# Kernel optimization log

Measured on AMD Instinct MI355X. Metric: run time of the kernel, lower is better.

Reference implementation:

```python
import jax, jax.numpy as jnp
import numpy as np

N = 100000
E = 1600000
IN_FT = 128
HID = 128
LEAK = 0.2  # GATConv default negative_slope


def _glorot(key, shape):
    fan_in, fan_out = shape[0], shape[-1]
    s = float(np.sqrt(6.0 / (fan_in + fan_out)))
    return jax.random.uniform(key, shape, jnp.float32, -s, s)


def setup_inputs() -> dict:
    key = jax.random.key(0)
    ks = jax.random.split(key, 12)
    return {
        "x": jax.random.normal(ks[0], (N, IN_FT), jnp.float32),
        "edge_index": jax.random.randint(ks[1], (2, E), 0, N, dtype=jnp.int64) if jax.config.jax_enable_x64 else jax.random.randint(ks[1], (2, E), 0, N, dtype=jnp.int32),
        "edge_weight": jax.random.uniform(ks[2], (E,), jnp.float32),
        "W1": _glorot(ks[3], (IN_FT, HID)),
        "a_src1": _glorot(ks[4], (HID, 1))[:, 0],
        "a_dst1": _glorot(ks[5], (HID, 1))[:, 0],
        "b1": jnp.zeros((HID,), jnp.float32),
        "W2": _glorot(ks[6], (HID, HID)),
        "a_src2": _glorot(ks[7], (HID, 1))[:, 0],
        "a_dst2": _glorot(ks[8], (HID, 1))[:, 0],
        "b2": jnp.zeros((HID,), jnp.float32),
    }


def _gat_layer(h_in, src, dst, n, W, a_src, a_dst, b):
    # h: [N, HID] dense projection
    h = h_in @ W
    # per-node attention halves, then edge-wise combine (classic GAT, 1 head)
    s_src = h @ a_src  # [N]
    s_dst = h @ a_dst  # [N]
    e = jax.nn.leaky_relu(s_src[src] + s_dst[dst], LEAK)  # [E+N]
    # softmax over incoming edges of each dst node (self-loops guarantee non-empty)
    m = jax.ops.segment_max(e, dst, num_segments=n)
    ex = jnp.exp(e - m[dst])
    denom = jax.ops.segment_sum(ex, dst, num_segments=n)
    alpha = ex / denom[dst]
    # scatter-aggregate messages alpha_ij * h_j
    out = jax.ops.segment_sum(alpha[:, None] * h[src], dst, num_segments=n)
    return out + b


def reference(x, edge_index, edge_weight, W1, a_src1, a_dst1, b1, W2, a_src2, a_dst2, b2):
    # edge_weight is accepted but unused: PyG GATConv with edge_dim=None ignores edge_attr.
    n = x.shape[0]
    loops = jnp.arange(n, dtype=edge_index.dtype)  # add_self_loops=True
    src = jnp.concatenate([edge_index[0], loops])
    dst = jnp.concatenate([edge_index[1], loops])
    x1 = jnp.tanh(_gat_layer(x, src, dst, n, W1, a_src1, a_dst1, b1))
    # dropout: identity in eval mode
    x2 = _gat_layer(x1, src, dst, n, W2, a_src2, a_dst2, b2)
    # update='max': elementwise max over stacked layer outputs
    return jnp.maximum(x1, x2)
```

## Files before the change

### kernel.cpp

```cpp
#include <hip/hip_runtime.h>
#include <math.h>

#define NN 100000
#define NE 1600000
#define EE 1700000
#define HD 128
#define NH (NN*HD)

#define BSH 8
#define NBUK 391
#define CAP 6144
#define EPB 4096
#define P1B ((EE + EPB - 1) / EPB)
#define GEMMB 1563

typedef _Float16 f16x8 __attribute__((ext_vector_type(8)));
typedef float    f32x4 __attribute__((ext_vector_type(4)));

__device__ __forceinline__ float fast_tanh(float x) {
    float e = __expf(2.f * x);
    return 1.f - 2.f * __builtin_amdgcn_rcpf(e + 1.f);
}

__global__ void wt12_kernel(const float* __restrict__ W1, const float* __restrict__ W2,
                            _Float16* __restrict__ Wt1, _Float16* __restrict__ Wt2) {
    int b = blockIdx.x;
    const float* W = (b < 64) ? W1 : W2;
    _Float16* Wt   = (b < 64) ? Wt1 : Wt2;
    int e = (b & 63) * 256 + threadIdx.x;
    int k = e >> 7, n = e & 127;
    Wt[n*HD + k] = (_Float16)W[e];
}

__launch_bounds__(256) __global__
void gemm_part_kernel(const float* __restrict__ A, const _Float16* __restrict__ Wt,
                      _Float16* __restrict__ H, const float* __restrict__ a_src,
                      const float* __restrict__ a_dst, float* __restrict__ s_src,
                      float* __restrict__ s_dst,
                      const int* __restrict__ ei, int* __restrict__ bucketCount,
                      unsigned* __restrict__ stage) {
    __shared__ __align__(16) char smem[HD*HD*2 + HD*8];
    int bid = blockIdx.x;
    int t = threadIdx.x;

    if (bid < GEMMB) {
        _Float16* Wl = (_Float16*)smem;
        float* asl = (float*)(smem + HD*HD*2);
        float* adl = asl + HD;
        #pragma unroll
        for (int i = 0; i < 8; ++i) {
            int f = t + 256*i;
            int n = f >> 4, slot = f & 15;
            int phys = n*16 + (slot ^ (n & 7));
            *(float4*)(Wl + (size_t)phys*8) = ((const float4*)Wt)[f];
        }
        if (t < HD) { asl[t] = a_src[t]; adl[t] = a_dst[t]; }
        __syncthreads();

        int wave = t >> 6, lane = t & 63;
        int row0 = bid*64 + wave*16;
        int h8   = lane >> 4;
        int col  = lane & 15;
        int arow = row0 + col; if (arow >= NN) arow = NN - 1;
        const float* Af = A + (size_t)arow*HD + h8*8;

        f32x4 acc[8];
        #pragma unroll
        for (int i = 0; i < 8; ++i) acc[i] = (f32x4){0.f,0.f,0.f,0.f};

        #pragma unroll
        for (int step = 0; step < 4; ++step) {
            float4 fa = *(const float4*)(Af + step*32);
            float4 fb = *(const float4*)(Af + step*32 + 4);
            f16x8 a = { (_Float16)fa.x, (_Float16)fa.y, (_Float16)fa.z, (_Float16)fa.w,
                        (_Float16)fb.x, (_Float16)fb.y, (_Float16)fb.z, (_Float16)fb.w };
            #pragma unroll
            for (int nt = 0; nt < 8; ++nt) {
                int n = nt*16 + col;
                int slot = step*4 + h8;
                f16x8 bfr = *(const f16x8*)(Wl + (size_t)(n*16 + (slot ^ (n & 7)))*8);
                acc[nt] = __builtin_amdgcn_mfma_f32_16x16x32_f16(a, bfr, acc[nt], 0, 0, 0);
            }
        }

        int orow0 = row0 + h8*4;
        #pragma unroll
        for (int nt = 0; nt < 8; ++nt) {
            int c = nt*16 + col;
            #pragma unroll
            for (int r = 0; r < 4; ++r) {
                int row = orow0 + r;
                if (row < NN) H[(size_t)row*HD + c] = (_Float16)acc[nt][r];
            }
        }

        float pS[4] = {0.f,0.f,0.f,0.f}, pD[4] = {0.f,0.f,0.f,0.f};
        #pragma unroll
        for (int nt = 0; nt < 8; ++nt) {
            float as_ = asl[nt*16 + col], ad_ = adl[nt*16 + col];
            #pragma unroll
            for (int r = 0; r < 4; ++r) { pS[r] += acc[nt][r]*as_; pD[r] += acc[nt][r]*ad_; }
        }
        #pragma unroll
        for (int off = 1; off < 16; off <<= 1) {
            #pragma unroll
            for (int r = 0; r < 4; ++r) {
                pS[r] += __shfl_xor(pS[r], off);
                pD[r] += __shfl_xor(pD[r], off);
            }
        }
        if (col == 0) {
            #pragma unroll
            for (int r = 0; r < 4; ++r) {
                int row = orow0 + r;
                if (row < NN) { s_src[row] = pS[r]; s_dst[row] = pD[r]; }
            }
        }
    } else if (ei) {
        int* hist = (int*)smem;
        int* base = hist + NBUK;
        for (int i = t; i < NBUK; i += 256) hist[i] = 0;
        __syncthreads();
        int pb = bid - GEMMB;
        int e0 = pb * EPB;
        int e1 = min(e0 + EPB, EE);
        for (int e = e0 + t; e < e1; e += 256) {
            int d = (e < NE) ? ei[NE + e] : e - NE;
            atomicAdd(&hist[d >> BSH], 1);
        }
        __syncthreads();
        for (int i = t; i < NBUK; i += 256) {
            base[i] = atomicAdd(&bucketCount[i], hist[i]);
            hist[i] = 0;
        }
        __syncthreads();
        for (int e = e0 + t; e < e1; e += 256) {
            int s, d;
            if (e < NE) { s = ei[e]; d = ei[NE + e]; } else { s = e - NE; d = s; }
            int b = d >> BSH;
            int pos = base[b] + atomicAdd(&hist[b], 1);
            if (pos < CAP)
                stage[(size_t)b * CAP + pos] = (unsigned)s | ((unsigned)(d & 255) << 20);
        }
    }
}

__launch_bounds__(256) __global__
void bucket_build_kernel(const unsigned* __restrict__ stage, const int* __restrict__ bucketCount,
                         int* __restrict__ row_ptr, int* __restrict__ csr_src,
                         int* __restrict__ degCount) {
    int b = blockIdx.x;
    int t = threadIdx.x;
    __shared__ int ldeg[256];
    __shared__ int loff[256];
    __shared__ int dhist[64];
    __shared__ int sbase;
    int c = 0;
    if (t < b) c = bucketCount[t];
    if (t + 256 < b) c += bucketCount[t + 256];
    loff[t] = c;
    ldeg[t] = 0;
    if (t < 64) dhist[t] = 0;
    __syncthreads();
    for (int off = 128; off >= 1; off >>= 1) {
        if (t < off) loff[t] += loff[t + off];
        __syncthreads();
    }
    if (t == 0) sbase = loff[0];
    __syncthreads();
    int cnt  = bucketCount[b];
    int base = sbase;
    const unsigned* sp = stage + (size_t)b * CAP;
    int n0 = b << BSH;
    for (int i = t; i < cnt; i += 256) atomicAdd(&ldeg[sp[i] >> 20], 1);
    __syncthreads();
    int v = ldeg[t];
    int n = n0 + t;
    if (n < NN) atomicAdd(&dhist[min(v, 63)], 1);
    loff[t] = v;
    __syncthreads();
    for (int off = 1; off < 256; off <<= 1) {
        int tmp = (t >= off) ? loff[t - off] : 0;
        __syncthreads();
        loff[t] += tmp;
        __syncthreads();
    }
    int excl = loff[t] - v;
    if (n < NN) row_ptr[n] = base + excl;
    if (b == NBUK - 1 && t == 0) row_ptr[NN] = EE;
    if (t < 64 && dhist[t]) atomicAdd(&degCount[t], dhist[t]);
    ldeg[t] = excl;
    __syncthreads();
    for (int i = t; i < cnt; i += 256) {
        unsigned p = sp[i];
        int lp = atomicAdd(&ldeg[p >> 20], 1);
        csr_src[base + lp] = (int)(p & 0xFFFFFu);
    }
}

__launch_bounds__(256) __global__
void perm_kernel(const int* __restrict__ row_ptr, const int* __restrict__ degCount,
                 int* __restrict__ degCursor, int* __restrict__ perm) {
    __shared__ int dbase[64], lhist[64], lbase[64];
    int t = threadIdx.x, n = blockIdx.x * 256 + t;
    if (t < 64) lhist[t] = 0;
    __syncthreads();
    int d = 0, myt = 0;
    if (n < NN) {
        int deg = row_ptr[n+1] - row_ptr[n];
        d = min(deg, 63);
        myt = atomicAdd(&lhist[d], 1);
    }
    __syncthreads();
    if (t < 64) lbase[t] = lhist[t] ? atomicAdd(&degCursor[t], lhist[t]) : 0;
    if (t == 0) {
        int run = 0;
        for (int i = 0; i < 64; ++i) { dbase[i] = run; run += degCount[i]; }
    }
    __syncthreads();
    if (n < NN) perm[dbase[d] + lbase[d] + myt] = n;
}

template<int LAYER>
__launch_bounds__(256) __global__
void gat_node_kernel(const int* __restrict__ perm, const int* __restrict__ row_ptr,
                     const int* __restrict__ csr_src,
                     const float* __restrict__ s_src, const float* __restrict__ s_dst,
                     const _Float16* __restrict__ Hh, const float* __restrict__ bias,
                     float* __restrict__ out) {
    int wid = (blockIdx.x * blockDim.x + threadIdx.x) >> 6;
    int lane = threadIdx.x & 63;
    int g = lane >> 4, l16 = lane & 15;
    int idx = wid*4 + g;
    if (idx >= NN) return;
    int n = perm[idx];
    int r0 = row_ptr[n], r1 = row_ptr[n+1];
    int last = r1 - 1;
    float sdv = s_dst[n];

    float denom = 0.f;
    float acc[8] = {0.f,0.f,0.f,0.f,0.f,0.f,0.f,0.f};

    int j = r0;
    int jB = min(j+1, last), jC = min(j+2, last), jD = min(j+3, last);
    int sA = csr_src[j],  sB = csr_src[jB], sC = csr_src[jC], sD = csr_src[jD];
    f16x8 hA = *(const f16x8*)(Hh + (unsigned)(sA << 7) + l16*8);
    f16x8 hB = *(const f16x8*)(Hh + (unsigned)(sB << 7) + l16*8);
    f16x8 hC = *(const f16x8*)(Hh + (unsigned)(sC << 7) + l16*8);
    f16x8 hD = *(const f16x8*)(Hh + (unsigned)(sD << 7) + l16*8);
    float vA = s_src[sA], vB = s_src[sB], vC = s_src[sC], vD = s_src[sD];

    while (true) {
        int jn = j + 4;
        bool more = jn < r1;
        int kj = more ? jn : r0;
        int kB = min(kj+1, last), kC = min(kj+2, last), kD = min(kj+3, last);
        int tA = csr_src[kj], tB = csr_src[kB], tC = csr_src[kC], tD = csr_src[kD];
        f16x8 nA = *(const f16x8*)(Hh + (unsigned)(tA << 7) + l16*8);
        f16x8 nB = *(const f16x8*)(Hh + (unsigned)(tB << 7) + l16*8);
        f16x8 nC = *(const f16x8*)(Hh + (unsigned)(tC << 7) + l16*8);
        f16x8 nD = *(const f16x8*)(Hh + (unsigned)(tD << 7) + l16*8);
        float uA = s_src[tA], uB = s_src[tB], uC = s_src[tC], uD = s_src[tD];

        float eA = vA + sdv, eB = vB + sdv, eC = vC + sdv, eD = vD + sdv;
        eA = eA > 0.f ? eA : 0.2f*eA;  eB = eB > 0.f ? eB : 0.2f*eB;
        eC = eC > 0.f ? eC : 0.2f*eC;  eD = eD > 0.f ? eD : 0.2f*eD;
        float wA = __expf(fminf(eA, 80.f));
        float wB = (j+1 < r1) ? __expf(fminf(eB, 80.f)) : 0.f;
        float wC = (j+2 < r1) ? __expf(fminf(eC, 80.f)) : 0.f;
        float wD = (j+3 < r1) ? __expf(fminf(eD, 80.f)) : 0.f;
        denom += (wA + wB) + (wC + wD);
        #pragma unroll
        for (int i = 0; i < 8; ++i)
            acc[i] += wA*(float)hA[i] + wB*(float)hB[i] + wC*(float)hC[i] + wD*(float)hD[i];

        if (!more) break;
        j = jn;
        sA = tA; sB = tB; sC = tC; sD = tD;
        hA = nA; hB = nB; hC = nC; hD = nD;
        vA = uA; vB = uB; vC = uC; vD = uD;
    }

    float inv = __builtin_amdgcn_rcpf(denom);
    float* op = out + (unsigned)(n << 7) + l16*8;
    float4 b0 = *(const float4*)(bias + l16*8);
    float4 b1 = *(const float4*)(bias + l16*8 + 4);
    float r[8];
    r[0]=acc[0]*inv+b0.x; r[1]=acc[1]*inv+b0.y; r[2]=acc[2]*inv+b0.z; r[3]=acc[3]*inv+b0.w;
    r[4]=acc[4]*inv+b1.x; r[5]=acc[5]*inv+b1.y; r[6]=acc[6]*inv+b1.z; r[7]=acc[7]*inv+b1.w;
    if (LAYER == 1) {
        #pragma unroll
        for (int i = 0; i < 8; ++i) r[i] = fast_tanh(r[i]);
    } else {
        float4 x0 = *(const float4*)op;
        float4 x1 = *(const float4*)(op + 4);
        r[0]=fmaxf(x0.x,r[0]); r[1]=fmaxf(x0.y,r[1]); r[2]=fmaxf(x0.z,r[2]); r[3]=fmaxf(x0.w,r[3]);
        r[4]=fmaxf(x1.x,r[4]); r[5]=fmaxf(x1.y,r[5]); r[6]=fmaxf(x1.z,r[6]); r[7]=fmaxf(x1.w,r[7]);
    }
    *(float4*)op       = make_float4(r[0],r[1],r[2],r[3]);
    *(float4*)(op + 4) = make_float4(r[4],r[5],r[6],r[7]);
}

extern "C" void kernel_launch(void* const* d_in, const int* in_sizes, int n_in,
                              void* d_out, int out_size, void* d_ws, size_t ws_size,
                              hipStream_t stream) {
    const float* x   = (const float*)d_in[0];
    const int*   ei  = (const int*)d_in[1];
    const float* W1  = (const float*)d_in[3];
    const float* as1 = (const float*)d_in[4];
    const float* ad1 = (const float*)d_in[5];
    const float* b1  = (const float*)d_in[6];
    const float* W2  = (const float*)d_in[7];
    const float* as2 = (const float*)d_in[8];
    const float* ad2 = (const float*)d_in[9];
    const float* b2  = (const float*)d_in[10];
    float* out = (float*)d_out;

    char* wsb = (char*)d_ws;
    _Float16* h   = (_Float16*)wsb;
    _Float16* Wt1 = h + NH;
    _Float16* Wt2 = Wt1 + HD*HD;
    float* ssrc   = (float*)(Wt2 + HD*HD);
    float* sdst   = ssrc + NN;
    int* row_ptr  = (int*)(sdst + NN);
    int* perm     = row_ptr + NN + 2;
    int* csr_src  = perm + NN;
    int* bucketCount = csr_src + EE;
    int* degCount    = bucketCount + NBUK;
    int* degCursor   = degCount + 64;
    unsigned* stage  = (unsigned*)(degCursor + 64 + 2);

    dim3 B(256);
    int node_blocks = NN / 16;

    hipMemsetAsync(bucketCount, 0, (NBUK + 128) * sizeof(int), stream);
    wt12_kernel<<<128, B, 0, stream>>>(W1, W2, Wt1, Wt2);

    gemm_part_kernel<<<GEMMB + P1B, B, 0, stream>>>(x, Wt1, h, as1, ad1, ssrc, sdst,
                                                    ei, bucketCount, stage);
    bucket_build_kernel<<<NBUK, B, 0, stream>>>(stage, bucketCount, row_ptr, csr_src, degCount);
    perm_kernel<<<NBUK, B, 0, stream>>>(row_ptr, degCount, degCursor, perm);

    gat_node_kernel<1><<<node_blocks, B, 0, stream>>>(perm, row_ptr, csr_src, ssrc, sdst, h, b1, out);

    gemm_part_kernel<<<GEMMB, B, 0, stream>>>(out, Wt2, h, as2, ad2, ssrc, sdst,
                                              nullptr, nullptr, nullptr);
    gat_node_kernel<2><<<node_blocks, B, 0, stream>>>(perm, row_ptr, csr_src, ssrc, sdst, h, b2, out);
}
```

Before: 267.1 us.

## Replace degree-sorted node permutation with persistent atomic-ticket work distribution

Drops the degree histogram, the perm_kernel launch and the degree-sorted node permutation. The aggregation kernel becomes persistent: 2048 blocks in which each wavefront claims groups of four nodes through a global atomic ticket counter. The software-pipelined prefetch of the next four neighbours is also replaced by a plain loop. This removes one kernel launch and the sorting passes, but nodes are now processed in natural order, so the four nodes sharing a wavefront can differ in degree, and the explicit load prefetch overlap is lost.

```diff
diff --git a/kernel.cpp b/kernel.cpp
--- a/kernel.cpp
+++ b/kernel.cpp
@@ -6,6 +6,7 @@
 #define EE 1700000
 #define HD 128
 #define NH (NN*HD)
+#define NQUAD (NN/4)
 
 #define BSH 8
 #define NBUK 391
@@ -147,20 +148,17 @@
 
 __launch_bounds__(256) __global__
 void bucket_build_kernel(const unsigned* __restrict__ stage, const int* __restrict__ bucketCount,
-                         int* __restrict__ row_ptr, int* __restrict__ csr_src,
-                         int* __restrict__ degCount) {
+                         int* __restrict__ row_ptr, int* __restrict__ csr_src) {
     int b = blockIdx.x;
     int t = threadIdx.x;
     __shared__ int ldeg[256];
     __shared__ int loff[256];
-    __shared__ int dhist[64];
     __shared__ int sbase;
     int c = 0;
     if (t < b) c = bucketCount[t];
     if (t + 256 < b) c += bucketCount[t + 256];
     loff[t] = c;
     ldeg[t] = 0;
-    if (t < 64) dhist[t] = 0;
     __syncthreads();
     for (int off = 128; off >= 1; off >>= 1) {
         if (t < off) loff[t] += loff[t + off];
@@ -175,8 +173,6 @@
     for (int i = t; i < cnt; i += 256) atomicAdd(&ldeg[sp[i] >> 20], 1);
     __syncthreads();
     int v = ldeg[t];
-    int n = n0 + t;
-    if (n < NN) atomicAdd(&dhist[min(v, 63)], 1);
     loff[t] = v;
     __syncthreads();
     for (int off = 1; off < 256; off <<= 1) {
@@ -186,9 +182,9 @@
         __syncthreads();
     }
     int excl = loff[t] - v;
+    int n = n0 + t;
     if (n < NN) row_ptr[n] = base + excl;
     if (b == NBUK - 1 && t == 0) row_ptr[NN] = EE;
-    if (t < 64 && dhist[t]) atomicAdd(&degCount[t], dhist[t]);
     ldeg[t] = excl;
     __syncthreads();
     for (int i = t; i < cnt; i += 256) {
@@ -198,107 +194,76 @@
     }
 }
 
-__launch_bounds__(256) __global__
-void perm_kernel(const int* __restrict__ row_ptr, const int* __restrict__ degCount,
-                 int* __restrict__ degCursor, int* __restrict__ perm) {
-    __shared__ int dbase[64], lhist[64], lbase[64];
-    int t = threadIdx.x, n = blockIdx.x * 256 + t;
-    if (t < 64) lhist[t] = 0;
-    __syncthreads();
-    int d = 0, myt = 0;
-    if (n < NN) {
-        int deg = row_ptr[n+1] - row_ptr[n];
-        d = min(deg, 63);
-        myt = atomicAdd(&lhist[d], 1);
-    }
-    __syncthreads();
-    if (t < 64) lbase[t] = lhist[t] ? atomicAdd(&degCursor[t], lhist[t]) : 0;
-    if (t == 0) {
-        int run = 0;
-        for (int i = 0; i < 64; ++i) { dbase[i] = run; run += degCount[i]; }
-    }
-    __syncthreads();
-    if (n < NN) perm[dbase[d] + lbase[d] + myt] = n;
-}
-
 template<int LAYER>
 __launch_bounds__(256) __global__
-void gat_node_kernel(const int* __restrict__ perm, const int* __restrict__ row_ptr,
-                     const int* __restrict__ csr_src,
+void gat_node_kernel(int* __restrict__ ticket,
+                     const int* __restrict__ row_ptr, const int* __restrict__ csr_src,
                      const float* __restrict__ s_src, const float* __restrict__ s_dst,
                      const _Float16* __restrict__ Hh, const float* __restrict__ bias,
                      float* __restrict__ out) {
-    int wid = (blockIdx.x * blockDim.x + threadIdx.x) >> 6;
     int lane = threadIdx.x & 63;
     int g = lane >> 4, l16 = lane & 15;
-    int idx = wid*4 + g;
-    if (idx >= NN) return;
-    int n = perm[idx];
-    int r0 = row_ptr[n], r1 = row_ptr[n+1];
-    int last = r1 - 1;
-    float sdv = s_dst[n];
-
-    float denom = 0.f;
-    float acc[8] = {0.f,0.f,0.f,0.f,0.f,0.f,0.f,0.f};
-
-    int j = r0;
-    int jB = min(j+1, last), jC = min(j+2, last), jD = min(j+3, last);
-    int sA = csr_src[j],  sB = csr_src[jB], sC = csr_src[jC], sD = csr_src[jD];
-    f16x8 hA = *(const f16x8*)(Hh + (unsigned)(sA << 7) + l16*8);
-    f16x8 hB = *(const f16x8*)(Hh + (unsigned)(sB << 7) + l16*8);
-    f16x8 hC = *(const f16x8*)(Hh + (unsigned)(sC << 7) + l16*8);
-    f16x8 hD = *(const f16x8*)(Hh + (unsigned)(sD << 7) + l16*8);
-    float vA = s_src[sA], vB = s_src[sB], vC = s_src[sC], vD = s_src[sD];
-
-    while (true) {
-        int jn = j + 4;
-        bool more = jn < r1;
-        int kj = more ? jn : r0;
-        int kB = min(kj+1, last), kC = min(kj+2, last), kD = min(kj+3, last);
-        int tA = csr_src[kj], tB = csr_src[kB], tC = csr_src[kC], tD = csr_src[kD];
-        f16x8 nA = *(const f16x8*)(Hh + (unsigned)(tA << 7) + l16*8);
-        f16x8 nB = *(const f16x8*)(Hh + (unsigned)(tB << 7) + l16*8);
-        f16x8 nC = *(const f16x8*)(Hh + (unsigned)(tC << 7) + l16*8);
-        f16x8 nD = *(const f16x8*)(Hh + (unsigned)(tD << 7) + l16*8);
-        float uA = s_src[tA], uB = s_src[tB], uC = s_src[tC], uD = s_src[tD];
-
-        float eA = vA + sdv, eB = vB + sdv, eC = vC + sdv, eD = vD + sdv;
-        eA = eA > 0.f ? eA : 0.2f*eA;  eB = eB > 0.f ? eB : 0.2f*eB;
-        eC = eC > 0.f ? eC : 0.2f*eC;  eD = eD > 0.f ? eD : 0.2f*eD;
-        float wA = __expf(fminf(eA, 80.f));
-        float wB = (j+1 < r1) ? __expf(fminf(eB, 80.f)) : 0.f;
-        float wC = (j+2 < r1) ? __expf(fminf(eC, 80.f)) : 0.f;
-        float wD = (j+3 < r1) ? __expf(fminf(eD, 80.f)) : 0.f;
-        denom += (wA + wB) + (wC + wD);
-        #pragma unroll
-        for (int i = 0; i < 8; ++i)
-            acc[i] += wA*(float)hA[i] + wB*(float)hB[i] + wC*(float)hC[i] + wD*(float)hD[i];
-
-        if (!more) break;
-        j = jn;
-        sA = tA; sB = tB; sC = tC; sD = tD;
-        hA = nA; hB = nB; hC = nC; hD = nD;
-        vA = uA; vB = uB; vC = uC; vD = uD;
-    }
-
-    float inv = __builtin_amdgcn_rcpf(denom);
-    float* op = out + (unsigned)(n << 7) + l16*8;
     float4 b0 = *(const float4*)(bias + l16*8);
     float4 b1 = *(const float4*)(bias + l16*8 + 4);
-    float r[8];
-    r[0]=acc[0]*inv+b0.x; r[1]=acc[1]*inv+b0.y; r[2]=acc[2]*inv+b0.z; r[3]=acc[3]*inv+b0.w;
-    r[4]=acc[4]*inv+b1.x; r[5]=acc[5]*inv+b1.y; r[6]=acc[6]*inv+b1.z; r[7]=acc[7]*inv+b1.w;
-    if (LAYER == 1) {
-        #pragma unroll
-        for (int i = 0; i < 8; ++i) r[i] = fast_tanh(r[i]);
-    } else {
-        float4 x0 = *(const float4*)op;
-        float4 x1 = *(const float4*)(op + 4);
-        r[0]=fmaxf(x0.x,r[0]); r[1]=fmaxf(x0.y,r[1]); r[2]=fmaxf(x0.z,r[2]); r[3]=fmaxf(x0.w,r[3]);
-        r[4]=fmaxf(x1.x,r[4]); r[5]=fmaxf(x1.y,r[5]); r[6]=fmaxf(x1.z,r[6]); r[7]=fmaxf(x1.w,r[7]);
-    }
-    *(float4*)op       = make_float4(r[0],r[1],r[2],r[3]);
-    *(float4*)(op + 4) = make_float4(r[4],r[5],r[6],r[7]);
+
+    while (true) {
+        int quad = 0;
+        if (lane == 0) quad = atomicAdd(ticket, 1);
+        quad = __builtin_amdgcn_readfirstlane(quad);
+        if (quad >= NQUAD) return;
+        int n = quad*4 + g;
+        int r0 = row_ptr[n], r1 = row_ptr[n+1];
+        int last = r1 - 1;
+        float sdv = s_dst[n];
+
+        float denom = 0.f;
+        float acc[8] = {0.f,0.f,0.f,0.f,0.f,0.f,0.f,0.f};
+
+        for (int j = r0; j < r1; j += 4) {
+            int jB = j+1 <= last ? j+1 : last;
+            int jC = j+2 <= last ? j+2 : last;
+            int jD = j+3 <= last ? j+3 : last;
+            int sA = csr_src[j];
+            int sB = csr_src[jB];
+            int sC = csr_src[jC];
+            int sD = csr_src[jD];
+            f16x8 hA = *(const f16x8*)(Hh + (unsigned)(sA << 7) + l16*8);
+            f16x8 hB = *(const f16x8*)(Hh + (unsigned)(sB << 7) + l16*8);
+            f16x8 hC = *(const f16x8*)(Hh + (unsigned)(sC << 7) + l16*8);
+            f16x8 hD = *(const f16x8*)(Hh + (unsigned)(sD << 7) + l16*8);
+            float eA = s_src[sA] + sdv;
+            float eB = s_src[sB] + sdv;
+            float eC = s_src[sC] + sdv;
+            float eD = s_src[sD] + sdv;
+            eA = eA > 0.f ? eA : 0.2f*eA;  eB = eB > 0.f ? eB : 0.2f*eB;
+            eC = eC > 0.f ? eC : 0.2f*eC;  eD = eD > 0.f ? eD : 0.2f*eD;
+            float wA = __expf(fminf(eA, 80.f));
+            float wB = (j+1 < r1) ? __expf(fminf(eB, 80.f)) : 0.f;
+            float wC = (j+2 < r1) ? __expf(fminf(eC, 80.f)) : 0.f;
+            float wD = (j+3 < r1) ? __expf(fminf(eD, 80.f)) : 0.f;
+            denom += (wA + wB) + (wC + wD);
+            #pragma unroll
+            for (int i = 0; i < 8; ++i)
+                acc[i] += wA*(float)hA[i] + wB*(float)hB[i] + wC*(float)hC[i] + wD*(float)hD[i];
+        }
+
+        float inv = __builtin_amdgcn_rcpf(denom);
+        float* op = out + (unsigned)(n << 7) + l16*8;
+        float r[8];
+        r[0]=acc[0]*inv+b0.x; r[1]=acc[1]*inv+b0.y; r[2]=acc[2]*inv+b0.z; r[3]=acc[3]*inv+b0.w;
+        r[4]=acc[4]*inv+b1.x; r[5]=acc[5]*inv+b1.y; r[6]=acc[6]*inv+b1.z; r[7]=acc[7]*inv+b1.w;
+        if (LAYER == 1) {
+            #pragma unroll
+            for (int i = 0; i < 8; ++i) r[i] = fast_tanh(r[i]);
+        } else {
+            float4 x0 = *(const float4*)op;
+            float4 x1 = *(const float4*)(op + 4);
+            r[0]=fmaxf(x0.x,r[0]); r[1]=fmaxf(x0.y,r[1]); r[2]=fmaxf(x0.z,r[2]); r[3]=fmaxf(x0.w,r[3]);
+            r[4]=fmaxf(x1.x,r[4]); r[5]=fmaxf(x1.y,r[5]); r[6]=fmaxf(x1.z,r[6]); r[7]=fmaxf(x1.w,r[7]);
+        }
+        *(float4*)op       = make_float4(r[0],r[1],r[2],r[3]);
+        *(float4*)(op + 4) = make_float4(r[4],r[5],r[6],r[7]);
+    }
 }
 
 extern "C" void kernel_launch(void* const* d_in, const int* in_sizes, int n_in,
@@ -323,27 +288,26 @@
     float* ssrc   = (float*)(Wt2 + HD*HD);
     float* sdst   = ssrc + NN;
     int* row_ptr  = (int*)(sdst + NN);
-    int* perm     = row_ptr + NN + 2;
-    int* csr_src  = perm + NN;
+    int* csr_src  = row_ptr + NN + 2;
     int* bucketCount = csr_src + EE;
-    int* degCount    = bucketCount + NBUK;
-    int* degCursor   = degCount + 64;
-    unsigned* stage  = (unsigned*)(degCursor + 64 + 2);
+    int* tickets     = bucketCount + NBUK;
+    unsigned* stage  = (unsigned*)(tickets + 8);
 
     dim3 B(256);
-    int node_blocks = NN / 16;
-
-    hipMemsetAsync(bucketCount, 0, (NBUK + 128) * sizeof(int), stream);
+    int agg_blocks = 2048;
+
+    hipMemsetAsync(bucketCount, 0, (NBUK + 8) * sizeof(int), stream);
     wt12_kernel<<<128, B, 0, stream>>>(W1, W2, Wt1, Wt2);
 
     gemm_part_kernel<<<GEMMB + P1B, B, 0, stream>>>(x, Wt1, h, as1, ad1, ssrc, sdst,
                                                     ei, bucketCount, stage);
-    bucket_build_kernel<<<NBUK, B, 0, stream>>>(stage, bucketCount, row_ptr, csr_src, degCount);
-    perm_kernel<<<NBUK, B, 0, stream>>>(row_ptr, degCount, degCursor, perm);
-
-    gat_node_kernel<1><<<node_blocks, B, 0, stream>>>(perm, row_ptr, csr_src, ssrc, sdst, h, b1, out);
+    bucket_build_kernel<<<NBUK, B, 0, stream>>>(stage, bucketCount, row_ptr, csr_src);
+
+    gat_node_kernel<1><<<agg_blocks, B, 0, stream>>>(tickets + 0, row_ptr, csr_src,
+                                                     ssrc, sdst, h, b1, out);
 
     gemm_part_kernel<<<GEMMB, B, 0, stream>>>(out, Wt2, h, as2, ad2, ssrc, sdst,
                                               nullptr, nullptr, nullptr);
-    gat_node_kernel<2><<<node_blocks, B, 0, stream>>>(perm, row_ptr, csr_src, ssrc, sdst, h, b2, out);
-}
+    gat_node_kernel<2><<<agg_blocks, B, 0, stream>>>(tickets + 1, row_ptr, csr_src,
+                                                     ssrc, sdst, h, b2, out);
+}
```

Measured after the change: 886.1 us. 3.32x slower.
